# Performance work log

Measured on AMD Instinct MI355X. Metric: run time of the kernel, lower is better.

Reference implementation:

```python
import jax, jax.numpy as jnp
import numpy as np
from jax import lax

DN = ('NCHW', 'OIHW', 'NCHW')

def _conv(x, w, pad):
    return lax.conv_general_dilated(x, w, (1, 1), pad, dimension_numbers=DN)

def _bn(x, p, eps=1e-5):
    # p: [4, C] rows = gamma, beta, mean, var ; inference-mode batchnorm
    g, b, m, v = p[0], p[1], p[2], p[3]
    scale = g / jnp.sqrt(v + eps)
    return (x - m[:, None, None]) * scale[:, None, None] + b[:, None, None]

def setup_inputs() -> dict:
    key = jax.random.key(0)
    ks = jax.random.split(key, 12)
    B, C, H, W = 16, 512, 56, 56
    mid = C // 2
    def bn_params(k):
        k1, k2, k3, k4 = jax.random.split(k, 4)
        g = 1.0 + 0.1 * jax.random.normal(k1, (mid,), jnp.float32)
        b = 0.1 * jax.random.normal(k2, (mid,), jnp.float32)
        m = 0.1 * jax.random.normal(k3, (mid,), jnp.float32)
        v = 0.5 + jax.random.uniform(k4, (mid,), jnp.float32)
        return jnp.stack([g, b, m, v])
    return {
        'x': jax.random.normal(ks[0], (B, C, H, W), jnp.float32),
        'w_main': 0.03 * jax.random.normal(ks[1], (mid, C, 3, 3), jnp.float32),
        'w_1x1': 0.05 * jax.random.normal(ks[2], (mid, C, 1, 1), jnp.float32),
        'w31': 0.05 * jax.random.normal(ks[3], (mid, C, 1, 1), jnp.float32),
        'bn31': bn_params(ks[4]),
        'w33': 0.05 * jax.random.normal(ks[5], (mid, mid, 3, 3), jnp.float32),
        'bn33': bn_params(ks[6]),
        'wa1': 0.05 * jax.random.normal(ks[7], (mid, C, 1, 1), jnp.float32),
        'bna1': bn_params(ks[8]),
        'bna2': bn_params(ks[9]),
        'fuse_weight': jnp.ones((4,), jnp.float32),
        'c_score': jax.random.normal(ks[10], (2 * C,), jnp.float32),
    }

def reference(x, w_main, w_1x1, w31, bn31, w33, bn33, wa1, bna1, bna2, fuse_weight, c_score):
    c = x.shape[1]
    # four branches (note: forward applies BN only inside the 3x3 and avg branches)
    acs_main = _conv(x * fuse_weight[0], w_main, 'SAME')
    acs_1x1 = _conv(x * fuse_weight[1], w_1x1, 'VALID')
    acs_3x3 = _bn(_conv(_bn(_conv(x * fuse_weight[2], w31, 'VALID'), bn31), w33, 'SAME'), bn33)
    avg_in = _bn(_conv(x * fuse_weight[3], wa1, 'VALID'), bna1)
    # AvgPool2d(k=3, s=1, p=1, count_include_pad=True)
    pooled = lax.reduce_window(avg_in, 0.0, lax.add, (1, 1, 3, 3), (1, 1, 1, 1),
                               [(0, 0), (0, 0), (1, 1), (1, 1)]) / 9.0
    acs_avg = _bn(pooled, bna2)
    out = jnp.concatenate([acs_main, acs_1x1, acs_3x3, acs_avg], axis=1)  # [B, 2c, H, W]
    # sparse 1x1 selection: output channel i = input channel ind[i] * sigmoid(c_score[ind[i]])
    _, ind = lax.top_k(c_score, c)
    scale = jax.nn.sigmoid(c_score)[ind]  # [c]
    out = out[:, ind] * scale[None, :, None, None]
    return out
```

## Files before the change

### kernel.cpp

```cpp
#include <hip/hip_runtime.h>
#include <hip/hip_bf16.h>
#include <cstdint>
#include <cstddef>

typedef _Float16 f16x8_t __attribute__((ext_vector_type(8)));
typedef float    f32x4_t __attribute__((ext_vector_type(4)));
typedef unsigned short u16x8_t __attribute__((ext_vector_type(8)));
typedef unsigned short u16x4_t __attribute__((ext_vector_type(4)));

__device__ __forceinline__ unsigned short f2h(float f) {
    return __builtin_bit_cast(unsigned short, (_Float16)f);
}
__device__ __forceinline__ float h2f(unsigned short h) {
    return (float)__builtin_bit_cast(_Float16, h);
}
__device__ __forceinline__ f16x8_t load_h8(const unsigned short* p) {
    u16x8_t r = *(const u16x8_t*)p;
    return __builtin_bit_cast(f16x8_t, r);
}

#define BATCH 16
#define CFULL 512
#define CMID  256
#define HW    3136
#define WDIM  56

#define PLANE_SH 2784
#define LDS_SHORTS (4 * 2784)

__global__ void prep_tabs(const float* __restrict__ cscore,
                          const float* __restrict__ bn31, const float* __restrict__ bn33,
                          const float* __restrict__ bna1, const float* __restrict__ bna2,
                          int* __restrict__ pos_tab, float* __restrict__ scale_tab,
                          float* __restrict__ bnab)
{
    __shared__ float s[1024];
    int t = threadIdx.x;
    s[t] = cscore[t];
    __syncthreads();
    float sj = s[t];
    int cnt = 0;
    for (int k = 0; k < 1024; ++k) {
        float sk = s[k];
        cnt += (sk > sj) || (sk == sj && k < t);
    }
    pos_tab[t]   = (cnt < 512) ? cnt : -1;
    scale_tab[t] = 1.0f / (1.0f + expf(-sj));

    if (t < 256) {
        const float* srcs[4] = {bn31, bn33, bna1, bna2};
        #pragma unroll
        for (int q = 0; q < 4; ++q) {
            const float* sp = srcs[q];
            float g = sp[t], b = sp[256 + t], m = sp[512 + t], v = sp[768 + t];
            float a = g * rsqrtf(v + 1e-5f);
            bnab[q * 512 + t]       = a;
            bnab[q * 512 + 256 + t] = b - m * a;
        }
    }
}

__global__ void prep_weights(const float* __restrict__ w_main, const float* __restrict__ w_1x1,
                             const float* __restrict__ w31, const float* __restrict__ wa1,
                             const float* __restrict__ w33, const float* __restrict__ fw,
                             unsigned short* __restrict__ Wcat,
                             unsigned short* __restrict__ Wmain,
                             unsigned short* __restrict__ W33r)
{
    int i = blockIdx.x * 256 + threadIdx.x;
    if (i < 393216) {
        int row = i >> 9, c = i & 511;
        float v;
        if (row < 256)      v = w_1x1[row * 512 + c] * fw[1];
        else if (row < 512) v = w31[(row - 256) * 512 + c] * fw[2];
        else                v = wa1[(row - 512) * 512 + c] * fw[3];
        Wcat[((c >> 5) * 768 + row) * 32 + (c & 31)] = f2h(v);
    } else if (i < 393216 + 1179648) {
        int j = i - 393216;
        int o = j / 4608, r = j % 4608, tap = r >> 9, c = r & 511;
        Wmain[(((c >> 5) * 9 + tap) * 256 + o) * 32 + (c & 31)] =
            f2h(w_main[(size_t)(o * 512 + c) * 9 + tap] * fw[0]);
    } else if (i < 2162688) {
        int j = i - 1572864;
        int o = j / 2304, r = j % 2304, tap = r >> 8, c = r & 255;
        W33r[(((c >> 5) * 9 + tap) * 256 + o) * 32 + (c & 31)] =
            f2h(w33[(size_t)(o * 256 + c) * 9 + tap]);
    }
}

__global__ void transpose_x(const float* __restrict__ x, unsigned short* __restrict__ xt)
{
    __shared__ unsigned short tile[64][65];
    int t = threadIdx.x;
    int hw0 = blockIdx.x * 64, c0 = blockIdx.y * 64, b = blockIdx.z;
    const float* xb = x + ((size_t)b * CFULL + c0) * HW + hw0;
    int hwL = t & 63, cL = t >> 6;
    #pragma unroll
    for (int i = 0; i < 16; ++i) {
        int c = cL + i * 4;
        tile[c][hwL] = f2h(xb[(size_t)c * HW + hwL]);
    }
    __syncthreads();
    int c8 = (t & 7) * 8, hw = t >> 3;
    #pragma unroll
    for (int i = 0; i < 2; ++i) {
        int hh = hw + i * 32;
        u16x8_t v;
        #pragma unroll
        for (int j = 0; j < 8; ++j) v[j] = tile[c8 + j][hh];
        *(u16x8_t*)(xt + ((size_t)b * HW + hw0 + hh) * CFULL + c0 + c8) = v;
    }
}

template<int CIN, int NTAP, int MODE>
__device__ __forceinline__ void conv_body(
    const unsigned short* __restrict__ X,
    const unsigned short* __restrict__ Wr,
    float* __restrict__ out,
    unsigned short* __restrict__ u_dst,
    unsigned short* __restrict__ avg_dst,
    const float* __restrict__ bnab,
    const int* __restrict__ pos_tab,
    const float* __restrict__ scale_tab,
    unsigned short* smem, int b, int ob, int pb)
{
    const int t    = threadIdx.x;
    const int lane = t & 63;
    const int wid  = t >> 6;
    const int wm = wid >> 1, wn = wid & 1;
    const int lr = lane & 15;
    const int ko = (lane >> 4) * 8;
    const int kqp = (lane >> 4) * PLANE_SH;
    const int row0 = pb * 4;

    const int o_wave = ob * 128 + wm * 64;
    const int p_wave = pb * 224 + wn * 112;

    int bofs[7];
    #pragma unroll
    for (int n = 0; n < 7; ++n) {
        int p = p_wave + n * 16 + lr;
        bofs[n] = kqp + ((p / WDIM - row0) * 58 + p % WDIM) * 8;
    }

    const int r_lo = (NTAP == 9) ? 0 : 1;
    const int nitems = ((NTAP == 9) ? 6 : 4) * 224;
    int  s_src[6];
    int  s_dst[6];
    bool s_val[6];
    #pragma unroll
    for (int i = 0; i < 6; ++i) {
        int idx = t + i * 256;
        bool act = idx < nitems;
        int r   = r_lo + idx / 224;
        int rm  = idx % 224;
        int col = rm >> 2, sub = rm & 3;
        int ir  = row0 + r - 1;
        s_val[i] = act && ((unsigned)ir < (unsigned)WDIM);
        s_src[i] = (ir * WDIM + col) * CIN + sub * 8;
        s_dst[i] = sub * PLANE_SH + (r * 58 + col + 1) * 8;
    }

    #pragma unroll
    for (int i = 0; i < 7; ++i) {
        int j = t + i * 256;
        if (j < LDS_SHORTS / 8)
            *(u16x8_t*)(smem + j * 8) = (u16x8_t){0, 0, 0, 0, 0, 0, 0, 0};
    }

    f32x4_t acc[4][7];
    #pragma unroll
    for (int m = 0; m < 4; ++m)
        #pragma unroll
        for (int n = 0; n < 7; ++n)
            acc[m][n] = (f32x4_t){0.f, 0.f, 0.f, 0.f};

    const int astep = (MODE == 1) ? 768 * 32 : 256 * 32;
    const unsigned short* am[4];
    #pragma unroll
    for (int m = 0; m < 4; ++m)
        am[m] = Wr + (size_t)(o_wave + m * 16 + lr) * 32 + ko;

    const unsigned short* xb = X + (size_t)b * HW * CIN;
    const int KCH = CIN / 32;

    for (int kch = 0; kch < KCH; ++kch) {
        __syncthreads();
        u16x8_t buf[6];
        #pragma unroll
        for (int i = 0; i < 6; ++i)
            if (s_val[i]) buf[i] = *(const u16x8_t*)(xb + s_src[i] + kch * 32);
        #pragma unroll
        for (int i = 0; i < 6; ++i)
            if (s_val[i]) *(u16x8_t*)(smem + s_dst[i]) = buf[i];
        __syncthreads();

        #pragma unroll
        for (int tap = 0; tap < NTAP; ++tap) {
            const int toff = (NTAP == 9) ? (((tap / 3) * 58 + tap % 3) * 8)
                                         : (59 * 8);
            f16x8_t af[4];
            #pragma unroll
            for (int m = 0; m < 4; ++m)
                af[m] = load_h8(am[m] + (size_t)(kch * NTAP + tap) * astep);
            f16x8_t bf[7];
            #pragma unroll
            for (int n = 0; n < 7; ++n)
                bf[n] = load_h8(smem + bofs[n] + toff);
            __builtin_amdgcn_s_setprio(1);
            #pragma unroll
            for (int m = 0; m < 4; ++m)
                #pragma unroll
                for (int n = 0; n < 7; ++n)
                    acc[m][n] = __builtin_amdgcn_mfma_f32_16x16x32_f16(af[m], bf[n], acc[m][n], 0, 0, 0);
            __builtin_amdgcn_s_setprio(0);
        }
    }

    const int fq = lane >> 4;
    const int seg = (MODE == 1) ? (ob >> 1) : 0;
    const bool bn_write = (MODE == 1) && (seg != 0);

    #pragma unroll
    for (int m = 0; m < 4; ++m) {
        const int orow = o_wave + m * 16 + fq * 4;
        #pragma unroll
        for (int n = 0; n < 7; ++n) {
            const int p = p_wave + n * 16 + lr;
            f32x4_t v = acc[m][n];
            if (bn_write) {
                const int lc0 = orow - seg * 256;
                const float* ab = (seg == 1) ? (bnab + 0 * 512) : (bnab + 2 * 512);
                unsigned short* dst = (seg == 1) ? u_dst : avg_dst;
                u16x4_t pk;
                #pragma unroll
                for (int j = 0; j < 4; ++j) {
                    float a = ab[lc0 + j], bb = ab[256 + lc0 + j];
                    pk[j] = f2h(a * v[j] + bb);
                }
                *(u16x4_t*)(dst + ((size_t)b * HW + p) * CMID + lc0) = pk;
            } else {
                const int cbase = (MODE == 0) ? 0 : ((MODE == 2) ? 512 : 256);
                #pragma unroll
                for (int j = 0; j < 4; ++j) {
                    int o = orow + j;
                    float val2 = v[j];
                    if (MODE == 2) val2 = bnab[512 + o] * val2 + bnab[512 + 256 + o];
                    int jc = cbase + o;
                    int pos = pos_tab[jc];
                    if (pos >= 0)
                        out[((size_t)b * CFULL + pos) * HW + p] = val2 * scale_tab[jc];
                }
            }
        }
    }
}

template<int CIN, int MODE>
__device__ __forceinline__ void conv_sched(
    const unsigned short* __restrict__ X,
    const unsigned short* __restrict__ Wr,
    float* __restrict__ out,
    const float* __restrict__ bnab,
    const int* __restrict__ pos_tab,
    const float* __restrict__ scale_tab,
    unsigned short* smem, int b, int ob, int pb)
{
    const int t    = threadIdx.x;
    const int lane = t & 63;
    const int wid  = t >> 6;
    const int wm = wid >> 1, wn = wid & 1;
    const int lr = lane & 15;
    const int ko = (lane >> 4) * 8;
    const int kqp = (lane >> 4) * PLANE_SH;
    const int row0 = pb * 4;

    const int o_wave = ob * 128 + wm * 64;
    const int p_wave = pb * 224 + wn * 112;

    int bofs[7];
    #pragma unroll
    for (int n = 0; n < 7; ++n) {
        int p = p_wave + n * 16 + lr;
        bofs[n] = kqp + ((p / WDIM - row0) * 58 + p % WDIM) * 8;
    }

    const int nitems = 6 * 224;
    const int dump_off = 2 * LDS_SHORTS + (t & 63) * 8 + (wid & 3) * 512;
    int s_src[6];
    int s_dst[6];
    #pragma unroll
    for (int i = 0; i < 6; ++i) {
        int idx = t + i * 256;
        int r   = idx / 224;
        int rm  = idx % 224;
        int col = rm >> 2, sub = rm & 3;
        int ir  = row0 + r - 1;
        bool v  = (idx < nitems) && ((unsigned)ir < (unsigned)WDIM);
        int ir_c = v ? ir : 0;
        s_src[i] = (ir_c * WDIM + col) * CIN + sub * 8;
        s_dst[i] = v ? (sub * PLANE_SH + (r * 58 + col + 1) * 8) : dump_off;
    }

    #pragma unroll
    for (int i = 0; i < 14; ++i) {
        int j = t + i * 256;
        if (j < 2 * LDS_SHORTS / 8)
            *(u16x8_t*)(smem + j * 8) = (u16x8_t){0, 0, 0, 0, 0, 0, 0, 0};
    }

    f32x4_t acc[4][7];
    #pragma unroll
    for (int m = 0; m < 4; ++m)
        #pragma unroll
        for (int n = 0; n < 7; ++n)
            acc[m][n] = (f32x4_t){0.f, 0.f, 0.f, 0.f};

    const int astep = 256 * 32;
    const unsigned short* am[4];
    #pragma unroll
    for (int m = 0; m < 4; ++m)
        am[m] = Wr + (size_t)(o_wave + m * 16 + lr) * 32 + ko;

    const unsigned short* xb = X + (size_t)b * HW * CIN;
    const int KCH = CIN / 32;
    const int NT = KCH * 9;

    f16x8_t af[3][4];

    u16x8_t sbuf[6];
    __syncthreads();
    #pragma unroll
    for (int i = 0; i < 6; ++i)
        sbuf[i] = *(const u16x8_t*)(xb + s_src[i]);
    asm volatile("s_waitcnt vmcnt(0)" ::: "memory");
    #pragma unroll
    for (int i = 0; i < 6; ++i)
        *(u16x8_t*)(smem + s_dst[i]) = sbuf[i];
    #pragma unroll
    for (int m = 0; m < 4; ++m)
        af[0][m] = load_h8(am[m]);
    #pragma unroll
    for (int m = 0; m < 4; ++m)
        af[1][m] = load_h8(am[m] + (size_t)1 * astep);
    asm volatile("s_waitcnt lgkmcnt(0)" ::: "memory");
    __builtin_amdgcn_s_barrier();

    #pragma unroll 1
    for (int kch = 0; kch < KCH; ++kch) {
        const unsigned short* rbuf = smem + (kch & 1) * LDS_SHORTS;
        unsigned short* wbuf = smem + ((kch + 1) & 1) * LDS_SHORTS;
        const int nk = (kch + 1 < KCH) ? (kch + 1) : 0;

        #pragma unroll
        for (int tap = 0; tap < 9; ++tap) {
            const int fill = (tap + 2) % 3;
            const int use  = tap % 3;
            int kt = kch * 9 + tap + 2;
            if (kt >= NT) kt -= NT;
            #pragma unroll
            for (int m = 0; m < 4; ++m)
                af[fill][m] = load_h8(am[m] + (size_t)kt * astep);
            if (tap == 7) {
                #pragma unroll
                for (int i = 0; i < 6; ++i)
                    sbuf[i] = *(const u16x8_t*)(xb + s_src[i] + nk * 32);
            }
            const int toff = ((tap / 3) * 58 + tap % 3) * 8;
            f16x8_t bf[7];
            #pragma unroll
            for (int n = 0; n < 7; ++n)
                bf[n] = load_h8(rbuf + bofs[n] + toff);
            if (tap < 7)
                asm volatile("s_waitcnt vmcnt(8) lgkmcnt(0)" ::: "memory");
            else
                asm volatile("s_waitcnt vmcnt(14) lgkmcnt(0)" ::: "memory");
            __builtin_amdgcn_sched_barrier(0);
            __builtin_amdgcn_s_setprio(1);
            #pragma unroll
            for (int m = 0; m < 4; ++m)
                #pragma unroll
                for (int n = 0; n < 7; ++n)
                    acc[m][n] = __builtin_amdgcn_mfma_f32_16x16x32_f16(af[use][m], bf[n], acc[m][n], 0, 0, 0);
            __builtin_amdgcn_s_setprio(0);
            __builtin_amdgcn_sched_barrier(0);
        }

        asm volatile("s_waitcnt vmcnt(4)" ::: "memory");
        #pragma unroll
        for (int i = 0; i < 6; ++i)
            *(u16x8_t*)(wbuf + s_dst[i]) = sbuf[i];
        asm volatile("s_waitcnt lgkmcnt(0)" ::: "memory");
        __builtin_amdgcn_s_barrier();
    }

    const int fq = lane >> 4;
    #pragma unroll
    for (int m = 0; m < 4; ++m) {
        const int orow = o_wave + m * 16 + fq * 4;
        #pragma unroll
        for (int n = 0; n < 7; ++n) {
            const int p = p_wave + n * 16 + lr;
            f32x4_t v = acc[m][n];
            const int cbase = (MODE == 0) ? 0 : 512;
            #pragma unroll
            for (int j = 0; j < 4; ++j) {
                int o = orow + j;
                float val2 = v[j];
                if (MODE == 2) val2 = bnab[512 + o] * val2 + bnab[512 + 256 + o];
                int jc = cbase + o;
                int pos = pos_tab[jc];
                if (pos >= 0)
                    out[((size_t)b * CFULL + pos) * HW + p] = val2 * scale_tab[jc];
            }
        }
    }
}

__global__ __launch_bounds__(256, 2)
void convK1(const unsigned short* __restrict__ X,
            const unsigned short* __restrict__ Wmain,
            const unsigned short* __restrict__ Wcat,
            float* __restrict__ out,
            unsigned short* __restrict__ u_dst,
            unsigned short* __restrict__ avg_dst,
            const float* __restrict__ bnab,
            const int* __restrict__ pos_tab,
            const float* __restrict__ scale_tab)
{
    __shared__ unsigned short smem[2 * LDS_SHORTS + 2048];
    const int id = blockIdx.x;
    const int xcd = id & 7, slot = id >> 3;
    if (slot < 56) {
        const int b = xcd + 8 * (slot / 28);
        const int u = slot % 28;
        conv_sched<512, 0>(X, Wmain, out, bnab, pos_tab, scale_tab,
                           smem, b, u / 14, u % 14);
    } else {
        const int g = slot - 56;
        const int b = xcd + 8 * (g / 84);
        const int u = g % 84;
        conv_body<512, 1, 1>(X, Wcat, out, u_dst, avg_dst, bnab,
                             pos_tab, scale_tab, smem, b, u / 14, u % 14);
    }
}

__global__ __launch_bounds__(256, 2)
void convK2(const unsigned short* __restrict__ U,
            const unsigned short* __restrict__ W33r,
            const unsigned short* __restrict__ avgin,
            float* __restrict__ out,
            const float* __restrict__ bnab,
            const int* __restrict__ pos_tab,
            const float* __restrict__ scale_tab)
{
    __shared__ unsigned short smem[2 * LDS_SHORTS + 2048];
    const int id = blockIdx.x;
    const int xcd = id & 7, slot = id >> 3;
    if (slot < 56) {
        const int b = xcd + 8 * (slot / 28);
        const int u = slot % 28;
        conv_sched<256, 2>(U, W33r, out, bnab, pos_tab, scale_tab,
                           smem, b, u / 14, u % 14);
    } else {
        const int q = slot - 56;
        const int b = xcd + 8 * (q / 56);
        const int h = q % 56;
        const int t = threadIdx.x;
        const int c0 = (t & 31) * 8;
        const int ws = t >> 5;
        const float* ab2 = bnab + 3 * 512;
        const unsigned short* ab_base = avgin + (size_t)b * HW * CMID;

        #pragma unroll
        for (int i = 0; i < 7; ++i) {
            int w = ws * 7 + i;
            float s[8];
            #pragma unroll
            for (int j = 0; j < 8; ++j) s[j] = 0.f;
            #pragma unroll
            for (int dh = -1; dh <= 1; ++dh) {
                int hh = h + dh;
                if ((unsigned)hh >= (unsigned)WDIM) continue;
                u16x8_t v = *(const u16x8_t*)(ab_base + (size_t)(hh * WDIM + w) * CMID + c0);
                #pragma unroll
                for (int j = 0; j < 8; ++j) s[j] += h2f(v[j]);
            }
            u16x8_t pk;
            #pragma unroll
            for (int j = 0; j < 8; ++j) pk[j] = f2h(s[j]);
            *(u16x8_t*)(smem + w * CMID + c0) = pk;
        }
        __syncthreads();

        #pragma unroll
        for (int i = 0; i < 7; ++i) {
            int w = ws * 7 + i;
            float s[8];
            #pragma unroll
            for (int j = 0; j < 8; ++j) s[j] = 0.f;
            #pragma unroll
            for (int dw = -1; dw <= 1; ++dw) {
                int ww = w + dw;
                if ((unsigned)ww >= (unsigned)WDIM) continue;
                u16x8_t v = *(const u16x8_t*)(smem + ww * CMID + c0);
                #pragma unroll
                for (int j = 0; j < 8; ++j) s[j] += h2f(v[j]);
            }
            const int p = h * WDIM + w;
            #pragma unroll
            for (int j = 0; j < 8; ++j) {
                int c = c0 + j;
                int jc = 768 + c;
                int pos = pos_tab[jc];
                if (pos >= 0) {
                    float val = (s[j] * (1.f / 9.f)) * ab2[c] + ab2[256 + c];
                    out[((size_t)b * CFULL + pos) * HW + p] = val * scale_tab[jc];
                }
            }
        }
    }
}

extern "C" void kernel_launch(void* const* d_in, const int* in_sizes, int n_in,
                              void* d_out, int out_size, void* d_ws, size_t ws_size,
                              hipStream_t stream) {
    (void)in_sizes; (void)n_in; (void)out_size; (void)ws_size;
    const float* x      = (const float*)d_in[0];
    const float* w_main = (const float*)d_in[1];
    const float* w_1x1  = (const float*)d_in[2];
    const float* w31    = (const float*)d_in[3];
    const float* bn31   = (const float*)d_in[4];
    const float* w33    = (const float*)d_in[5];
    const float* bn33   = (const float*)d_in[6];
    const float* wa1    = (const float*)d_in[7];
    const float* bna1   = (const float*)d_in[8];
    const float* bna2   = (const float*)d_in[9];
    const float* fw     = (const float*)d_in[10];
    const float* cscore = (const float*)d_in[11];
    float* out = (float*)d_out;

    char* ws = (char*)d_ws;
    unsigned short* x_nhwc = (unsigned short*)(ws);
    unsigned short* u_nhwc = (unsigned short*)(ws + 51380224);
    unsigned short* avgin  = (unsigned short*)(ws + 77070336);
    unsigned short* Wcat   = (unsigned short*)(ws + 102760448);
    unsigned short* Wmain  = (unsigned short*)(ws + 103546880);
    unsigned short* W33r   = (unsigned short*)(ws + 105906176);
    float*          bnab   = (float*)        (ws + 107085824);
    int*            pos_tab= (int*)          (ws + 107094016);
    float*          scl_tab= (float*)        (ws + 107098112);

    dim3 blk(256);

    prep_tabs<<<dim3(1), dim3(1024), 0, stream>>>(cscore, bn31, bn33, bna1, bna2,
                                                  pos_tab, scl_tab, bnab);
    prep_weights<<<dim3(8448), blk, 0, stream>>>(w_main, w_1x1, w31, wa1, w33, fw,
                                                 Wcat, Wmain, W33r);
    transpose_x<<<dim3(49, 8, 16), blk, 0, stream>>>(x, x_nhwc);

    convK1<<<dim3(1792), blk, 0, stream>>>(x_nhwc, Wmain, Wcat, out,
                                           u_nhwc, avgin, bnab, pos_tab, scl_tab);

    convK2<<<dim3(1344), blk, 0, stream>>>(u_nhwc, W33r, avgin,
                                           out, bnab, pos_tab, scl_tab);
}
```

Baseline: 394.5 us.

## Split convK2 into smaller 128-thread blocks with half-size spatial tiles

```diff
diff --git a/kernel.cpp b/kernel.cpp
--- a/kernel.cpp
+++ b/kernel.cpp
@@ -27,6 +27,9 @@
 
 #define PLANE_SH 2784
 #define LDS_SHORTS (4 * 2784)
+
+#define PLANE2_SH 1856
+#define LDS2_SHORTS (4 * 1856)
 
 __global__ void prep_tabs(const float* __restrict__ cscore,
                           const float* __restrict__ bn31, const float* __restrict__ bn33,
@@ -417,6 +420,164 @@
     }
 }
 
+template<int CIN, int MODE>
+__device__ __forceinline__ void conv_sched2(
+    const unsigned short* __restrict__ X,
+    const unsigned short* __restrict__ Wr,
+    float* __restrict__ out,
+    const float* __restrict__ bnab,
+    const int* __restrict__ pos_tab,
+    const float* __restrict__ scale_tab,
+    unsigned short* smem, int b, int ob, int pb)
+{
+    const int t    = threadIdx.x;
+    const int lane = t & 63;
+    const int wid  = t >> 6;
+    const int lr = lane & 15;
+    const int ko = (lane >> 4) * 8;
+    const int kqp = (lane >> 4) * PLANE2_SH;
+    const int row0 = pb * 2;
+
+    const int o_wave = ob * 128 + wid * 64;
+    const int p_wave = pb * 112;
+
+    int bofs[7];
+    #pragma unroll
+    for (int n = 0; n < 7; ++n) {
+        int p = p_wave + n * 16 + lr;
+        bofs[n] = kqp + ((p / WDIM - row0) * 58 + p % WDIM) * 8;
+    }
+
+    const int nitems = 4 * 224;
+    const int dump_off = 2 * LDS2_SHORTS + lane * 8 + wid * 512;
+    int s_src[7];
+    int s_dst[7];
+    #pragma unroll
+    for (int i = 0; i < 7; ++i) {
+        int idx = t + i * 128;
+        int r   = idx / 224;
+        int rm  = idx % 224;
+        int col = rm >> 2, sub = rm & 3;
+        int ir  = row0 + r - 1;
+        bool v  = (idx < nitems) && ((unsigned)ir < (unsigned)WDIM);
+        int ir_c = v ? ir : 0;
+        s_src[i] = (ir_c * WDIM + col) * CIN + sub * 8;
+        s_dst[i] = v ? (sub * PLANE2_SH + (r * 58 + col + 1) * 8) : dump_off;
+    }
+
+    #pragma unroll
+    for (int i = 0; i < 15; ++i) {
+        int j = t + i * 128;
+        if (j < 2 * LDS2_SHORTS / 8)
+            *(u16x8_t*)(smem + j * 8) = (u16x8_t){0, 0, 0, 0, 0, 0, 0, 0};
+    }
+
+    f32x4_t acc[4][7];
+    #pragma unroll
+    for (int m = 0; m < 4; ++m)
+        #pragma unroll
+        for (int n = 0; n < 7; ++n)
+            acc[m][n] = (f32x4_t){0.f, 0.f, 0.f, 0.f};
+
+    const int astep = 256 * 32;
+    const unsigned short* am[4];
+    #pragma unroll
+    for (int m = 0; m < 4; ++m)
+        am[m] = Wr + (size_t)(o_wave + m * 16 + lr) * 32 + ko;
+
+    const unsigned short* xb = X + (size_t)b * HW * CIN;
+    const int KCH = CIN / 32;
+    const int NT = KCH * 9;
+
+    f16x8_t af[3][4];
+
+    u16x8_t sbuf[7];
+    __syncthreads();
+    #pragma unroll
+    for (int i = 0; i < 7; ++i)
+        sbuf[i] = *(const u16x8_t*)(xb + s_src[i]);
+    asm volatile("s_waitcnt vmcnt(0)" ::: "memory");
+    #pragma unroll
+    for (int i = 0; i < 7; ++i)
+        *(u16x8_t*)(smem + s_dst[i]) = sbuf[i];
+    #pragma unroll
+    for (int m = 0; m < 4; ++m)
+        af[0][m] = load_h8(am[m]);
+    #pragma unroll
+    for (int m = 0; m < 4; ++m)
+        af[1][m] = load_h8(am[m] + (size_t)1 * astep);
+    asm volatile("s_waitcnt lgkmcnt(0)" ::: "memory");
+    __builtin_amdgcn_s_barrier();
+
+    #pragma unroll 1
+    for (int kch = 0; kch < KCH; ++kch) {
+        const unsigned short* rbuf = smem + (kch & 1) * LDS2_SHORTS;
+        unsigned short* wbuf = smem + ((kch + 1) & 1) * LDS2_SHORTS;
+        const int nk = (kch + 1 < KCH) ? (kch + 1) : 0;
+
+        #pragma unroll
+        for (int tap = 0; tap < 9; ++tap) {
+            const int fill = (tap + 2) % 3;
+            const int use  = tap % 3;
+            int kt = kch * 9 + tap + 2;
+            if (kt >= NT) kt -= NT;
+            #pragma unroll
+            for (int m = 0; m < 4; ++m)
+                af[fill][m] = load_h8(am[m] + (size_t)kt * astep);
+            if (tap == 7) {
+                #pragma unroll
+                for (int i = 0; i < 7; ++i)
+                    sbuf[i] = *(const u16x8_t*)(xb + s_src[i] + nk * 32);
+            }
+            const int toff = ((tap / 3) * 58 + tap % 3) * 8;
+            f16x8_t bf[7];
+            #pragma unroll
+            for (int n = 0; n < 7; ++n)
+                bf[n] = load_h8(rbuf + bofs[n] + toff);
+            if (tap < 7)
+                asm volatile("s_waitcnt vmcnt(8) lgkmcnt(0)" ::: "memory");
+            else
+                asm volatile("s_waitcnt vmcnt(15) lgkmcnt(0)" ::: "memory");
+            __builtin_amdgcn_sched_barrier(0);
+            __builtin_amdgcn_s_setprio(1);
+            #pragma unroll
+            for (int m = 0; m < 4; ++m)
+                #pragma unroll
+                for (int n = 0; n < 7; ++n)
+                    acc[m][n] = __builtin_amdgcn_mfma_f32_16x16x32_f16(af[use][m], bf[n], acc[m][n], 0, 0, 0);
+            __builtin_amdgcn_s_setprio(0);
+            __builtin_amdgcn_sched_barrier(0);
+        }
+
+        asm volatile("s_waitcnt vmcnt(4)" ::: "memory");
+        #pragma unroll
+        for (int i = 0; i < 7; ++i)
+            *(u16x8_t*)(wbuf + s_dst[i]) = sbuf[i];
+        asm volatile("s_waitcnt lgkmcnt(0)" ::: "memory");
+        __builtin_amdgcn_s_barrier();
+    }
+
+    const int fq = lane >> 4;
+    #pragma unroll
+    for (int m = 0; m < 4; ++m) {
+        const int orow = o_wave + m * 16 + fq * 4;
+        #pragma unroll
+        for (int n = 0; n < 7; ++n) {
+            const int p = p_wave + n * 16 + lr;
+            f32x4_t v = acc[m][n];
+            #pragma unroll
+            for (int j = 0; j < 4; ++j) {
+                int o = orow + j;
+                float val2 = bnab[512 + o] * v[j] + bnab[512 + 256 + o];
+                int jc = 512 + o;
+                int pos = pos_tab[jc];
+                if (pos >= 0)
+                    out[((size_t)b * CFULL + pos) * HW + p] = val2 * scale_tab[jc];
+            }
+        }
+    }
+}
+
 __global__ __launch_bounds__(256, 2)
 void convK1(const unsigned short* __restrict__ X,
             const unsigned short* __restrict__ Wmain,
@@ -445,7 +606,7 @@
     }
 }
 
-__global__ __launch_bounds__(256, 2)
+__global__ __launch_bounds__(128, 2)
 void convK2(const unsigned short* __restrict__ U,
             const unsigned short* __restrict__ W33r,
             const unsigned short* __restrict__ avgin,
@@ -454,16 +615,16 @@
             const int* __restrict__ pos_tab,
             const float* __restrict__ scale_tab)
 {
-    __shared__ unsigned short smem[2 * LDS_SHORTS + 2048];
+    __shared__ unsigned short smem[2 * LDS2_SHORTS + 1024];
     const int id = blockIdx.x;
     const int xcd = id & 7, slot = id >> 3;
-    if (slot < 56) {
-        const int b = xcd + 8 * (slot / 28);
-        const int u = slot % 28;
-        conv_sched<256, 2>(U, W33r, out, bnab, pos_tab, scale_tab,
-                           smem, b, u / 14, u % 14);
+    if (slot < 112) {
+        const int b = xcd + 8 * (slot / 56);
+        const int u = slot % 56;
+        conv_sched2<256, 2>(U, W33r, out, bnab, pos_tab, scale_tab,
+                            smem, b, u / 28, u % 28);
     } else {
-        const int q = slot - 56;
+        const int q = slot - 112;
         const int b = xcd + 8 * (q / 56);
         const int h = q % 56;
         const int t = threadIdx.x;
@@ -473,8 +634,8 @@
         const unsigned short* ab_base = avgin + (size_t)b * HW * CMID;
 
         #pragma unroll
-        for (int i = 0; i < 7; ++i) {
-            int w = ws * 7 + i;
+        for (int i = 0; i < 14; ++i) {
+            int w = ws * 14 + i;
             float s[8];
             #pragma unroll
             for (int j = 0; j < 8; ++j) s[j] = 0.f;
@@ -494,8 +655,8 @@
         __syncthreads();
 
         #pragma unroll
-        for (int i = 0; i < 7; ++i) {
-            int w = ws * 7 + i;
+        for (int i = 0; i < 14; ++i) {
+            int w = ws * 14 + i;
             float s[8];
             #pragma unroll
             for (int j = 0; j < 8; ++j) s[j] = 0.f;
@@ -551,17 +712,15 @@
     int*            pos_tab= (int*)          (ws + 107094016);
     float*          scl_tab= (float*)        (ws + 107098112);
 
-    dim3 blk(256);
-
     prep_tabs<<<dim3(1), dim3(1024), 0, stream>>>(cscore, bn31, bn33, bna1, bna2,
                                                   pos_tab, scl_tab, bnab);
-    prep_weights<<<dim3(8448), blk, 0, stream>>>(w_main, w_1x1, w31, wa1, w33, fw,
-                                                 Wcat, Wmain, W33r);
-    transpose_x<<<dim3(49, 8, 16), blk, 0, stream>>>(x, x_nhwc);
-
-    convK1<<<dim3(1792), blk, 0, stream>>>(x_nhwc, Wmain, Wcat, out,
-                                           u_nhwc, avgin, bnab, pos_tab, scl_tab);
-
-    convK2<<<dim3(1344), blk, 0, stream>>>(u_nhwc, W33r, avgin,
-                                           out, bnab, pos_tab, scl_tab);
-}
+    prep_weights<<<dim3(8448), dim3(256), 0, stream>>>(w_main, w_1x1, w31, wa1, w33, fw,
+                                                       Wcat, Wmain, W33r);
+    transpose_x<<<dim3(49, 8, 16), dim3(256), 0, stream>>>(x, x_nhwc);
+
+    convK1<<<dim3(1792), dim3(256), 0, stream>>>(x_nhwc, Wmain, Wcat, out,
+                                                 u_nhwc, avgin, bnab, pos_tab, scl_tab);
+
+    convK2<<<dim3(1792), dim3(128), 0, stream>>>(u_nhwc, W33r, avgin,
+                                                 out, bnab, pos_tab, scl_tab);
+}
```

New measurement: 410.8 us. 1.04x slower.
